# Kernel optimization log

Measured on AMD Instinct MI355X. Metric: run time of the kernel, lower is better.

The kernel has to match this reference:

```python
import jax, jax.numpy as jnp
import numpy as np

EMBED = 768
HEADS = 12
HEAD_DIM = EMBED // HEADS
HIDDEN = 4 * EMBED
EPS = 1e-5


def setup_inputs() -> dict:
    key = jax.random.key(0)
    ks = jax.random.split(key, 12)
    s = lambda fan_in: 1.0 / np.sqrt(fan_in)
    return {
        "x": jax.random.normal(ks[0], (4, 2048, EMBED), dtype=jnp.float32),
        "ln1_g": jnp.ones((EMBED,), jnp.float32),
        "ln1_b": jnp.zeros((EMBED,), jnp.float32),
        "qkv_w": jax.random.normal(ks[1], (EMBED, 3 * EMBED), jnp.float32) * s(EMBED),
        "qkv_b": jnp.zeros((3 * EMBED,), jnp.float32),
        "proj_w": jax.random.normal(ks[2], (EMBED, EMBED), jnp.float32) * s(EMBED),
        "proj_b": jnp.zeros((EMBED,), jnp.float32),
        "ln2_g": jnp.ones((EMBED,), jnp.float32),
        "ln2_b": jnp.zeros((EMBED,), jnp.float32),
        "fc1_w": jax.random.normal(ks[3], (EMBED, HIDDEN), jnp.float32) * s(EMBED),
        "fc1_b": jnp.zeros((HIDDEN,), jnp.float32),
        "fc2_w": jax.random.normal(ks[4], (HIDDEN, EMBED), jnp.float32) * s(HIDDEN),
        "fc2_b": jnp.zeros((EMBED,), jnp.float32),
    }


def _layernorm(x, g, b):
    mu = jnp.mean(x, axis=-1, keepdims=True)
    var = jnp.var(x, axis=-1, keepdims=True)
    return (x - mu) * jax.lax.rsqrt(var + EPS) * g + b


def reference(x, ln1_g, ln1_b, qkv_w, qkv_b, proj_w, proj_b,
              ln2_g, ln2_b, fc1_w, fc1_b, fc2_w, fc2_b):
    B, N, C = x.shape
    # --- attention (pre-LN) ---
    xn = _layernorm(x, ln1_g, ln1_b)
    qkv = xn @ qkv_w + qkv_b                       # [B,N,3C]
    qkv = qkv.reshape(B, N, 3, HEADS, HEAD_DIM)
    q, k, v = jnp.moveaxis(qkv, 2, 0)              # each [B,N,H,D]
    q = jnp.swapaxes(q, 1, 2)                      # [B,H,N,D]
    k = jnp.swapaxes(k, 1, 2)
    v = jnp.swapaxes(v, 1, 2)
    scale = HEAD_DIM ** -0.5
    attn = jax.nn.softmax(jnp.einsum('bhnd,bhmd->bhnm', q, k) * scale, axis=-1)
    out = jnp.einsum('bhnm,bhmd->bhnd', attn, v)   # [B,H,N,D]
    out = jnp.swapaxes(out, 1, 2).reshape(B, N, C)
    out = out @ proj_w + proj_b
    x = x + out
    # --- MLP (pre-LN) ---
    xn2 = _layernorm(x, ln2_g, ln2_b)
    h = jax.nn.gelu(xn2 @ fc1_w + fc1_b, approximate=False)
    x = x + (h @ fc2_w + fc2_b)
    return x
```

## Files before the change

### kernel.cpp

```cpp
#include <hip/hip_runtime.h>

typedef unsigned short ushort_t;
typedef __attribute__((ext_vector_type(8))) unsigned short ushort8;
typedef __attribute__((ext_vector_type(4))) unsigned short ushort4v;
typedef __attribute__((ext_vector_type(2))) unsigned int uint2v;
typedef __attribute__((ext_vector_type(4))) unsigned int uint4v;
typedef __attribute__((ext_vector_type(4))) float f32x4;
typedef __attribute__((ext_vector_type(16))) float f32x16;
typedef __attribute__((ext_vector_type(8))) __bf16 bf16x8;

#define DEVFN static __device__ __forceinline__

DEVFN unsigned short f2bf(float f) {
    unsigned int u = __builtin_bit_cast(unsigned int, f);
    u += 0x7FFFu + ((u >> 16) & 1u);
    return (unsigned short)(u >> 16);
}

DEVFN bf16x8 ldsfrag(const ushort_t* p) {
    ushort8 u = *reinterpret_cast<const ushort8*>(p);
    return __builtin_bit_cast(bf16x8, u);
}

DEVFN bf16x8 ldg8(const ushort_t* p) {
    ushort8 u = *reinterpret_cast<const ushort8*>(p);
    return __builtin_bit_cast(bf16x8, u);
}

DEVFN f32x4 mfma16(bf16x8 a, bf16x8 b, f32x4 c) {
    return __builtin_amdgcn_mfma_f32_16x16x32_bf16(a, b, c, 0, 0, 0);
}

DEVFN f32x16 mfma32(bf16x8 a, bf16x8 b, f32x16 c) {
    return __builtin_amdgcn_mfma_f32_32x32x16_bf16(a, b, c, 0, 0, 0);
}

DEVFN void gl2lds16(const ushort_t* g, ushort_t* l) {
    __builtin_amdgcn_global_load_lds(
        (const __attribute__((address_space(1))) unsigned int*)g,
        (__attribute__((address_space(3))) unsigned int*)l, 16, 0, 0);
}

DEVFN unsigned int cvtpk(float lo, float hi) {
    unsigned int r;
    asm("v_cvt_pk_bf16_f32 %0, %1, %2" : "=v"(r) : "v"(lo), "v"(hi));
    return r;
}

DEVFN void permswap(unsigned int& a, unsigned int& b) {
    asm("v_permlane32_swap_b32 %0, %1" : "+v"(a), "+v"(b));
}

DEVFN float gelu_fast(float v) {
    const float a = 0.7978845608f * v * fmaf(0.044715f, v * v, 1.0f);
    const float e = __builtin_amdgcn_exp2f(2.885390082f * a);
    const float th = 1.0f - 2.0f * __builtin_amdgcn_rcpf(e + 1.0f);
    return 0.5f * v * (1.0f + th);
}

__global__ __launch_bounds__(256) void prep_kernel(
    const float* __restrict__ qkv_w, const float* __restrict__ proj_w,
    const float* __restrict__ fc1_w, const float* __restrict__ fc2_w,
    ushort_t* __restrict__ qkv_wt, ushort_t* __restrict__ proj_wt,
    ushort_t* __restrict__ fc1_wt, ushort_t* __restrict__ fc2_wt,
    const float* __restrict__ x, const float* __restrict__ ln1_g,
    const float* __restrict__ ln1_b, ushort_t* __restrict__ xb) {
    __shared__ float t[32][33];
    const int bid = blockIdx.x;
    const int tid = threadIdx.x;

    if (bid >= 6912) {
        const int row = bid - 6912;
        const float* xr = x + (size_t)row * 768;
        float v0 = xr[tid], v1 = xr[tid + 256], v2 = xr[tid + 512];
        float s = v0 + v1 + v2;
        float q = v0 * v0 + v1 * v1 + v2 * v2;
        for (int d = 32; d; d >>= 1) {
            s += __shfl_down(s, d);
            q += __shfl_down(q, d);
        }
        float* red = &t[0][0];
        const int w = tid >> 6, lane = tid & 63;
        if (lane == 0) { red[w] = s; red[4 + w] = q; }
        __syncthreads();
        if (tid == 0) {
            float ts = red[0] + red[1] + red[2] + red[3];
            float tq = red[4] + red[5] + red[6] + red[7];
            float mu = ts * (1.0f / 768.0f);
            float var = tq * (1.0f / 768.0f) - mu * mu;
            red[0] = mu;
            red[1] = rsqrtf(var + 1e-5f);
        }
        __syncthreads();
        const float mu = red[0], rs = red[1];
        ushort_t* orow = xb + (size_t)row * 768;
        orow[tid]       = f2bf((v0 - mu) * rs * ln1_g[tid]       + ln1_b[tid]);
        orow[tid + 256] = f2bf((v1 - mu) * rs * ln1_g[tid + 256] + ln1_b[tid + 256]);
        orow[tid + 512] = f2bf((v2 - mu) * rs * ln1_g[tid + 512] + ln1_b[tid + 512]);
        return;
    }

    const float* in; ushort_t* out; int K, N, n0, k0;
    if (bid < 1728)      { in = qkv_w;  out = qkv_wt;  K = 768;  N = 2304;
                           n0 = (bid % 72) * 32;  k0 = (bid / 72) * 32; }
    else if (bid < 2304) { const int r = bid - 1728; in = proj_w; out = proj_wt;
                           K = 768;  N = 768;
                           n0 = (r % 24) * 32;    k0 = (r / 24) * 32; }
    else if (bid < 4608) { const int r = bid - 2304; in = fc1_w;  out = fc1_wt;
                           K = 768;  N = 3072;
                           n0 = (r % 96) * 32;    k0 = (r / 96) * 32; }
    else                 { const int r = bid - 4608; in = fc2_w;  out = fc2_wt;
                           K = 3072; N = 768;
                           n0 = (r % 24) * 32;    k0 = (r / 24) * 32; }
    const int tx = tid & 31, ty = tid >> 5;
    for (int j = 0; j < 4; j++)
        t[ty + 8 * j][tx] = in[(size_t)(k0 + ty + 8 * j) * N + n0 + tx];
    __syncthreads();
    for (int j = 0; j < 4; j++)
        out[(size_t)(n0 + ty + 8 * j) * K + k0 + tx] = f2bf(t[tx][ty + 8 * j]);
}

__global__ __launch_bounds__(256) void ln_kernel(const float* __restrict__ x,
                                                 const float* __restrict__ g,
                                                 const float* __restrict__ bta,
                                                 ushort_t* __restrict__ out) {
    const int row = blockIdx.x;
    const int tid = threadIdx.x;
    const float* xr = x + (size_t)row * 768;
    float v0 = xr[tid], v1 = xr[tid + 256], v2 = xr[tid + 512];
    float s = v0 + v1 + v2;
    float q = v0 * v0 + v1 * v1 + v2 * v2;
    for (int d = 32; d; d >>= 1) {
        s += __shfl_down(s, d);
        q += __shfl_down(q, d);
    }
    __shared__ float red[8];
    const int w = tid >> 6, lane = tid & 63;
    if (lane == 0) { red[w] = s; red[4 + w] = q; }
    __syncthreads();
    if (tid == 0) {
        float ts = red[0] + red[1] + red[2] + red[3];
        float tq = red[4] + red[5] + red[6] + red[7];
        float mu = ts * (1.0f / 768.0f);
        float var = tq * (1.0f / 768.0f) - mu * mu;
        red[0] = mu;
        red[1] = rsqrtf(var + 1e-5f);
    }
    __syncthreads();
    const float mu = red[0], rs = red[1];
    ushort_t* orow = out + (size_t)row * 768;
    orow[tid]       = f2bf((v0 - mu) * rs * g[tid]       + bta[tid]);
    orow[tid + 256] = f2bf((v1 - mu) * rs * g[tid + 256] + bta[tid + 256]);
    orow[tid + 512] = f2bf((v2 - mu) * rs * g[tid + 512] + bta[tid + 512]);
}

enum { EPI_QKV = 0, EPI_RES = 1, EPI_GELU = 2 };

template <int EPI, int BN, int BK>
__global__ __launch_bounds__(256) void gemm_kernel(
    const ushort_t* __restrict__ A, const ushort_t* __restrict__ BT,
    const float* __restrict__ bias, const float* __restrict__ resid,
    float* __restrict__ outf, ushort_t* __restrict__ outb,
    ushort_t* __restrict__ vtout, int M, int N, int K) {
    constexpr int NT = BN / 32;
    constexpr int SL = BK / 8;
    constexpr int SM = SL - 1;
    constexpr int RPI = 64 / SL;
    constexpr int AI = 128 / RPI / 4;
    constexpr int BI = BN / RPI / 4;
    __shared__ __align__(16) ushort_t As[2][128 * BK];
    __shared__ __align__(16) ushort_t Bs[2][BN * BK];
    const int id = blockIdx.x;
    const int nbn = gridDim.x >> 6;
    const int p = id >> 3;
    const int bn = p % nbn;
    const int bm = (id & 7) * 8 + p / nbn;
    const int tid = threadIdx.x;
    const int lane = tid & 63, w = tid >> 6;
    const int wm = (w >> 1) * 64, wn = (w & 1) * (BN / 2);
    const int l15 = lane & 15, l4 = lane >> 4;

    const int srow = lane / SL;
    const int scol = ((lane & SM) ^ (srow & SM)) * 8;
    const ushort_t* gA = A + (size_t)(bm * 128 + w * (AI * RPI) + srow) * K + scol;
    const ushort_t* gB = BT + (size_t)(bn * BN + w * (BI * RPI) + srow) * K + scol;

    const int swm = l15 & SM;
    int aoff[BK / 32], boff[BK / 32];
#pragma unroll
    for (int kk = 0; kk < BK / 32; kk++) {
        aoff[kk] = (wm + l15) * BK + ((((kk << 2) | l4) ^ swm) * 8);
        boff[kk] = (wn + l15) * BK + ((((kk << 2) | l4) ^ swm) * 8);
    }

    f32x4 acc[4][NT] = {};

    auto stage = [&](int k0, int buf) {
#pragma unroll
        for (int i = 0; i < AI; i++)
            gl2lds16(gA + k0 + i * RPI * K, &As[buf][(w * AI + i) * 512]);
#pragma unroll
        for (int i = 0; i < BI; i++)
            gl2lds16(gB + k0 + i * RPI * K, &Bs[buf][(w * BI + i) * 512]);
    };

    stage(0, 0);
    __syncthreads();
    int cur = 0;
    for (int k0 = 0; k0 < K; k0 += BK) {
        if (k0 + BK < K) stage(k0 + BK, cur ^ 1);
#pragma unroll
        for (int kk = 0; kk < BK / 32; kk++) {
            bf16x8 af[4], bfr[NT];
#pragma unroll
            for (int mt = 0; mt < 4; mt++)
                af[mt] = ldsfrag(As[cur] + aoff[kk] + mt * 16 * BK);
#pragma unroll
            for (int nt = 0; nt < NT; nt++)
                bfr[nt] = ldsfrag(Bs[cur] + boff[kk] + nt * 16 * BK);
#pragma unroll
            for (int mt = 0; mt < 4; mt++)
#pragma unroll
                for (int nt = 0; nt < NT; nt++)
                    acc[mt][nt] = mfma16(bfr[nt], af[mt], acc[mt][nt]);
        }
        __syncthreads();
        cur ^= 1;
    }

#pragma unroll
    for (int nt = 0; nt < NT; nt++) {
        const int gc0 = bn * BN + wn + nt * 16 + l4 * 4;
        const f32x4 bi = *reinterpret_cast<const f32x4*>(bias + gc0);
#pragma unroll
        for (int mt = 0; mt < 4; mt++) {
            const int gr = bm * 128 + wm + mt * 16 + l15;
            f32x4 v = acc[mt][nt] + bi;
            if constexpr (EPI == EPI_QKV) {
                if (gc0 < 768) v *= 0.18033688011f;
                if (gc0 >= 1536) {
                    const int d = gc0 - 1536;
                    const int h = d >> 6, dh = d & 63;
                    const int b = gr >> 11, tl = gr & 2047;
                    ushort_t* vrow = vtout + ((size_t)((b * 12 + h) * 64 + dh)) * 2048 + tl;
                    vrow[0]        = f2bf(v[0]);
                    vrow[2048]     = f2bf(v[1]);
                    vrow[2 * 2048] = f2bf(v[2]);
                    vrow[3 * 2048] = f2bf(v[3]);
                } else {
                    uint2v o;
                    o[0] = cvtpk(v[0], v[1]);
                    o[1] = cvtpk(v[2], v[3]);
                    *reinterpret_cast<uint2v*>(outb + (size_t)gr * N + gc0) = o;
                }
            } else if constexpr (EPI == EPI_RES) {
                const f32x4 rsd = *reinterpret_cast<const f32x4*>(resid + (size_t)gr * N + gc0);
                *reinterpret_cast<f32x4*>(outf + (size_t)gr * N + gc0) = v + rsd;
            } else {
                f32x4 gl;
#pragma unroll
                for (int r = 0; r < 4; r++) gl[r] = gelu_fast(v[r]);
                uint2v o;
                o[0] = cvtpk(gl[0], gl[1]);
                o[1] = cvtpk(gl[2], gl[3]);
                *reinterpret_cast<uint2v*>(outb + (size_t)gr * N + gc0) = o;
            }
        }
    }
}

__global__ __launch_bounds__(256, 4) void attn_kernel(const ushort_t* __restrict__ qkv,
                                                      const ushort_t* __restrict__ vt,
                                                      ushort_t* __restrict__ out) {
    __shared__ __align__(16) ushort_t Kb[2][4096];
    __shared__ __align__(16) ushort_t Vb[2][4096];

    const int bid = blockIdx.x;
    const int nid = (bid & 7) * 96 + (bid >> 3);
    const int qt = nid & 15;
    const int bh = nid >> 4;
    const int b = bh / 12, h = bh % 12;
    const int tid = threadIdx.x;
    const int lane = tid & 63, w = tid >> 6;
    const int l31 = lane & 31, hi = lane >> 5;

    const ushort_t* qrow = qkv + (size_t)(b * 2048 + qt * 128 + w * 32 + l31) * 2304
                               + h * 64 + hi * 8;
    bf16x8 qf[4];
#pragma unroll
    for (int ks = 0; ks < 4; ks++) qf[ks] = ldg8(qrow + ks * 16);

    ushort8 onesu;
#pragma unroll
    for (int i = 0; i < 8; i++) onesu[i] = 0x3F80;
    const bf16x8 ones = __builtin_bit_cast(bf16x8, onesu);

    const int jr0 = w * 16 + (lane >> 3);
    const int jr1 = jr0 + 8;
    const int c0 = ((lane & 7) ^ (jr0 & 7)) * 8;
    const int c1 = ((lane & 7) ^ (jr1 & 7)) * 8;
    const ushort_t* kg0 = qkv + (size_t)(b * 2048 + jr0) * 2304 + 768 + h * 64 + c0;
    const ushort_t* kg1 = qkv + (size_t)(b * 2048 + jr1) * 2304 + 768 + h * 64 + c1;
    const ushort_t* vg0 = vt + (size_t)(bh * 64 + jr0) * 2048 + c0;
    const ushort_t* vg1 = vt + (size_t)(bh * 64 + jr1) * 2048 + c1;

    const int sw7 = lane & 7;
    int fo[4];
#pragma unroll
    for (int s = 0; s < 4; s++) fo[s] = l31 * 64 + ((((s << 1) | hi) ^ sw7) * 8);

    f32x16 oacc0 = {}, oacc1 = {};
    f32x16 lacc = {};

    gl2lds16(kg0, &Kb[0][w * 1024]);
    gl2lds16(kg1, &Kb[0][w * 1024 + 512]);
    gl2lds16(vg0, &Vb[0][w * 1024]);
    gl2lds16(vg1, &Vb[0][w * 1024 + 512]);
    __syncthreads();

    for (int kt = 0; kt < 32; kt++) {
        const int cur = kt & 1;
        if (kt < 31) {
            const size_t ko = (size_t)(kt + 1) * 64 * 2304;
            const int vo = (kt + 1) * 64;
            gl2lds16(kg0 + ko, &Kb[cur ^ 1][w * 1024]);
            gl2lds16(kg1 + ko, &Kb[cur ^ 1][w * 1024 + 512]);
            gl2lds16(vg0 + vo, &Vb[cur ^ 1][w * 1024]);
            gl2lds16(vg1 + vo, &Vb[cur ^ 1][w * 1024 + 512]);
        }
        const ushort_t* kb = Kb[cur];
        const ushort_t* vb = Vb[cur];

        f32x16 sA = {}, sB = {};
        __builtin_amdgcn_s_setprio(1);
#pragma unroll
        for (int ks = 0; ks < 4; ks++) {
            const bf16x8 k0 = ldsfrag(kb + fo[ks]);
            const bf16x8 k1 = ldsfrag(kb + fo[ks] + 2048);
            sA = mfma32(k0, qf[ks], sA);
            sB = mfma32(k1, qf[ks], sB);
        }
        __builtin_amdgcn_s_setprio(0);

        bf16x8 pf[4];
#pragma unroll
        for (int blk = 0; blk < 2; blk++) {
            const f32x16& sv = blk ? sB : sA;
            unsigned int wd[8];
#pragma unroll
            for (int g = 0; g < 4; g++) {
                const float e0 = __builtin_amdgcn_exp2f(sv[4 * g + 0]);
                const float e1 = __builtin_amdgcn_exp2f(sv[4 * g + 1]);
                const float e2 = __builtin_amdgcn_exp2f(sv[4 * g + 2]);
                const float e3 = __builtin_amdgcn_exp2f(sv[4 * g + 3]);
                wd[2 * g]     = cvtpk(e0, e1);
                wd[2 * g + 1] = cvtpk(e2, e3);
            }
            permswap(wd[0], wd[2]);
            permswap(wd[1], wd[3]);
            permswap(wd[4], wd[6]);
            permswap(wd[5], wd[7]);
            uint4v flo, fhi;
            flo[0] = wd[0]; flo[1] = wd[1]; flo[2] = wd[2]; flo[3] = wd[3];
            fhi[0] = wd[4]; fhi[1] = wd[5]; fhi[2] = wd[6]; fhi[3] = wd[7];
            pf[2 * blk]     = __builtin_bit_cast(bf16x8, flo);
            pf[2 * blk + 1] = __builtin_bit_cast(bf16x8, fhi);
        }

        __builtin_amdgcn_s_setprio(1);
#pragma unroll
        for (int s = 0; s < 4; s++) {
            const bf16x8 v0 = ldsfrag(vb + fo[s]);
            const bf16x8 v1 = ldsfrag(vb + fo[s] + 2048);
            oacc0 = mfma32(v0, pf[s], oacc0);
            oacc1 = mfma32(v1, pf[s], oacc1);
            lacc = mfma32(ones, pf[s], lacc);
        }
        __builtin_amdgcn_s_setprio(0);
        __syncthreads();
    }

    const float linv = __builtin_amdgcn_rcpf(lacc[0]);

    ushort_t* orow = out + (size_t)(b * 2048 + qt * 128 + w * 32 + l31) * 768 + h * 64;
#pragma unroll
    for (int dblk = 0; dblk < 2; dblk++) {
        const f32x16& ov = dblk ? oacc1 : oacc0;
#pragma unroll
        for (int g = 0; g < 4; g++) {
            const int d0 = dblk * 32 + 8 * g + 4 * hi;
            ushort4v o;
#pragma unroll
            for (int r = 0; r < 4; r++) o[r] = f2bf(ov[4 * g + r] * linv);
            *reinterpret_cast<ushort4v*>(orow + d0) = o;
        }
    }
}

extern "C" void kernel_launch(void* const* d_in, const int* in_sizes, int n_in,
                              void* d_out, int out_size, void* d_ws, size_t ws_size,
                              hipStream_t stream) {
    const float* x      = (const float*)d_in[0];
    const float* ln1_g  = (const float*)d_in[1];
    const float* ln1_b  = (const float*)d_in[2];
    const float* qkv_w  = (const float*)d_in[3];
    const float* qkv_b  = (const float*)d_in[4];
    const float* proj_w = (const float*)d_in[5];
    const float* proj_b = (const float*)d_in[6];
    const float* ln2_g  = (const float*)d_in[7];
    const float* ln2_b  = (const float*)d_in[8];
    const float* fc1_w  = (const float*)d_in[9];
    const float* fc1_b  = (const float*)d_in[10];
    const float* fc2_w  = (const float*)d_in[11];
    const float* fc2_b  = (const float*)d_in[12];
    float* out = (float*)d_out;

    char* ws = (char*)d_ws;
    ushort_t* qkv_wt  = (ushort_t*)(ws);
    ushort_t* proj_wt = (ushort_t*)(ws + 3538944);
    ushort_t* fc1_wt  = (ushort_t*)(ws + 4718592);
    ushort_t* fc2_wt  = (ushort_t*)(ws + 9437184);
    ushort_t* xb      = (ushort_t*)(ws + 14155776);
    ushort_t* aob     = (ushort_t*)(ws + 26738688);
    ushort_t* qkvb    = (ushort_t*)(ws + 39321600);
    ushort_t* vtb     = (ushort_t*)(ws + 77070336);
    ushort_t* hb      = (ushort_t*)(ws + 39321600);

    dim3 blk(256);

    prep_kernel<<<dim3(15104), blk, 0, stream>>>(qkv_w, proj_w, fc1_w, fc2_w,
                                                 qkv_wt, proj_wt, fc1_wt, fc2_wt,
                                                 x, ln1_g, ln1_b, xb);
    gemm_kernel<EPI_QKV, 128, 32><<<dim3(18 * 64), blk, 0, stream>>>(
        xb, qkv_wt, qkv_b, nullptr, nullptr, qkvb, vtb, 8192, 2304, 768);
    attn_kernel<<<dim3(768), blk, 0, stream>>>(qkvb, vtb, aob);
    gemm_kernel<EPI_RES, 64, 64><<<dim3(12 * 64), blk, 0, stream>>>(
        aob, proj_wt, proj_b, x, out, nullptr, nullptr, 8192, 768, 768);
    ln_kernel<<<8192, blk, 0, stream>>>(out, ln2_g, ln2_b, xb);
    gemm_kernel<EPI_GELU, 128, 32><<<dim3(24 * 64), blk, 0, stream>>>(
        xb, fc1_wt, fc1_b, nullptr, nullptr, hb, nullptr, 8192, 3072, 768);
    gemm_kernel<EPI_RES, 64, 64><<<dim3(12 * 64), blk, 0, stream>>>(
        hb, fc2_wt, fc2_b, out, out, nullptr, nullptr, 8192, 768, 3072);
}
```

Before: 270.7 us.

## Add triple-buffered LDS pipeline with vmcnt waits and MFMA priority to GEMMs

Adds an NBUF template parameter and a three-stage LDS ring buffer path for the BN=128/BK=32 GEMMs (QKV and FC1). Each step waits on vmcnt so that one stage's loads stay in flight, uses a single barrier per k-step, and issues loads two tiles ahead. MFMA issue is wrapped in s_setprio to favour the math wave. The extra buffer raises LDS use per block, which may reduce occupancy, and the hand-written waitcnt depends on the exact number of global-to-LDS loads per stage.

```diff
diff --git a/kernel.cpp b/kernel.cpp
--- a/kernel.cpp
+++ b/kernel.cpp
@@ -156,7 +156,7 @@
 
 enum { EPI_QKV = 0, EPI_RES = 1, EPI_GELU = 2 };
 
-template <int EPI, int BN, int BK>
+template <int EPI, int BN, int BK, int NBUF>
 __global__ __launch_bounds__(256) void gemm_kernel(
     const ushort_t* __restrict__ A, const ushort_t* __restrict__ BT,
     const float* __restrict__ bias, const float* __restrict__ resid,
@@ -168,8 +168,8 @@
     constexpr int RPI = 64 / SL;
     constexpr int AI = 128 / RPI / 4;
     constexpr int BI = BN / RPI / 4;
-    __shared__ __align__(16) ushort_t As[2][128 * BK];
-    __shared__ __align__(16) ushort_t Bs[2][BN * BK];
+    __shared__ __align__(16) ushort_t As[NBUF][128 * BK];
+    __shared__ __align__(16) ushort_t Bs[NBUF][BN * BK];
     const int id = blockIdx.x;
     const int nbn = gridDim.x >> 6;
     const int p = id >> 3;
@@ -204,28 +204,57 @@
             gl2lds16(gB + k0 + i * RPI * K, &Bs[buf][(w * BI + i) * 512]);
     };
 
-    stage(0, 0);
-    __syncthreads();
-    int cur = 0;
-    for (int k0 = 0; k0 < K; k0 += BK) {
-        if (k0 + BK < K) stage(k0 + BK, cur ^ 1);
-#pragma unroll
-        for (int kk = 0; kk < BK / 32; kk++) {
+    if constexpr (NBUF == 2) {
+        stage(0, 0);
+        __syncthreads();
+        int cur = 0;
+        for (int k0 = 0; k0 < K; k0 += BK) {
+            if (k0 + BK < K) stage(k0 + BK, cur ^ 1);
+#pragma unroll
+            for (int kk = 0; kk < BK / 32; kk++) {
+                bf16x8 af[4], bfr[NT];
+#pragma unroll
+                for (int mt = 0; mt < 4; mt++)
+                    af[mt] = ldsfrag(As[cur] + aoff[kk] + mt * 16 * BK);
+#pragma unroll
+                for (int nt = 0; nt < NT; nt++)
+                    bfr[nt] = ldsfrag(Bs[cur] + boff[kk] + nt * 16 * BK);
+#pragma unroll
+                for (int mt = 0; mt < 4; mt++)
+#pragma unroll
+                    for (int nt = 0; nt < NT; nt++)
+                        acc[mt][nt] = mfma16(bfr[nt], af[mt], acc[mt][nt]);
+            }
+            __syncthreads();
+            cur ^= 1;
+        }
+    } else {
+        static_assert(BK == 32 && BN == 128, "3-buf tuned for BN=128/BK=32");
+        const int nk = K / BK;
+        stage(0, 0);
+        stage(BK, 1);
+        for (int t = 0; t < nk; ++t) {
+            if (t + 1 < nk) asm volatile("s_waitcnt vmcnt(4)" ::: "memory");
+            else            asm volatile("s_waitcnt vmcnt(0)" ::: "memory");
+            __builtin_amdgcn_s_barrier();
+            if (t + 2 < nk) stage((t + 2) * BK, (t + 2) % 3);
+            const ushort_t* Ab = As[t % 3];
+            const ushort_t* Bb = Bs[t % 3];
             bf16x8 af[4], bfr[NT];
 #pragma unroll
             for (int mt = 0; mt < 4; mt++)
-                af[mt] = ldsfrag(As[cur] + aoff[kk] + mt * 16 * BK);
+                af[mt] = ldsfrag(Ab + aoff[0] + mt * 16 * BK);
 #pragma unroll
             for (int nt = 0; nt < NT; nt++)
-                bfr[nt] = ldsfrag(Bs[cur] + boff[kk] + nt * 16 * BK);
+                bfr[nt] = ldsfrag(Bb + boff[0] + nt * 16 * BK);
+            __builtin_amdgcn_s_setprio(1);
 #pragma unroll
             for (int mt = 0; mt < 4; mt++)
 #pragma unroll
                 for (int nt = 0; nt < NT; nt++)
                     acc[mt][nt] = mfma16(bfr[nt], af[mt], acc[mt][nt]);
-        }
-        __syncthreads();
-        cur ^= 1;
+            __builtin_amdgcn_s_setprio(0);
+        }
     }
 
 #pragma unroll
@@ -431,14 +460,14 @@
     prep_kernel<<<dim3(15104), blk, 0, stream>>>(qkv_w, proj_w, fc1_w, fc2_w,
                                                  qkv_wt, proj_wt, fc1_wt, fc2_wt,
                                                  x, ln1_g, ln1_b, xb);
-    gemm_kernel<EPI_QKV, 128, 32><<<dim3(18 * 64), blk, 0, stream>>>(
+    gemm_kernel<EPI_QKV, 128, 32, 3><<<dim3(18 * 64), blk, 0, stream>>>(
         xb, qkv_wt, qkv_b, nullptr, nullptr, qkvb, vtb, 8192, 2304, 768);
     attn_kernel<<<dim3(768), blk, 0, stream>>>(qkvb, vtb, aob);
-    gemm_kernel<EPI_RES, 64, 64><<<dim3(12 * 64), blk, 0, stream>>>(
+    gemm_kernel<EPI_RES, 64, 64, 2><<<dim3(12 * 64), blk, 0, stream>>>(
         aob, proj_wt, proj_b, x, out, nullptr, nullptr, 8192, 768, 768);
     ln_kernel<<<8192, blk, 0, stream>>>(out, ln2_g, ln2_b, xb);
-    gemm_kernel<EPI_GELU, 128, 32><<<dim3(24 * 64), blk, 0, stream>>>(
+    gemm_kernel<EPI_GELU, 128, 32, 3><<<dim3(24 * 64), blk, 0, stream>>>(
         xb, fc1_wt, fc1_b, nullptr, nullptr, hb, nullptr, 8192, 3072, 768);
-    gemm_kernel<EPI_RES, 64, 64><<<dim3(12 * 64), blk, 0, stream>>>(
+    gemm_kernel<EPI_RES, 64, 64, 2><<<dim3(12 * 64), blk, 0, stream>>>(
         hb, fc2_wt, fc2_b, out, out, nullptr, nullptr, 8192, 768, 3072);
 }
```

Measured after the change: 270.1 us. No clear change (-0.2%).
